# Optimization experiments

Hardware: AMD Instinct MI355X
Metric: run time of the kernel (lower is better)

Reference implementation:

```python
import jax, jax.numpy as jnp
import numpy as np

R = 0.5  # init kwarg r; reduction='mean'
N = 8192


def setup_inputs() -> dict:
    key = jax.random.key(0)
    k1, k2, k3 = jax.random.split(key, 3)
    pred = jax.random.normal(k1, (N, 1), dtype=jnp.float32)
    time = jax.random.uniform(k2, (N,), dtype=jnp.float32) * 100.0  # survival times
    event = jax.random.randint(k3, (N,), 0, 2).astype(jnp.float32)  # censoring indicator in {0,1}
    target = jnp.stack([time, event], axis=1)  # [N, 2]
    return {"pred": pred, "target": target}


def reference(pred, target):
    p = pred.squeeze(-1)            # [n]
    time = target[:, 0]             # [n]
    event = target[:, 1]            # [n]

    diff = p - time
    diff = jnp.where(event == 0, jnp.maximum(diff, 0.0), diff)
    regression_loss = jnp.mean(diff * diff)

    # ranking branch over all n^2 ordered pairs (i=index2 slow, j=index1 fast):
    # valid pair iff time[j] > time[i] and event[i] == 1
    mask = (time[None, :] > time[:, None]) & (event[:, None] == 1)  # [n, n] bool
    hinge = jnp.maximum(1.0 - p[None, :] + p[:, None], 0.0)         # [n, n]
    cnt = jnp.maximum(mask.sum(), 1).astype(jnp.float32)            # dynamic pair count -> masked mean
    ranking_loss = jnp.sum(jnp.where(mask, hinge * hinge, 0.0)) / cnt

    return R * ranking_loss + (1.0 - R) * regression_loss
```

## Files before the change

### kernel.cpp

```cpp
#include <hip/hip_runtime.h>

#define BLK 256
#define ITILE 256
#define KJ 2
#define JTILE (BLK * KJ)

__global__ __launch_bounds__(BLK) void svm_partial(
    const float* __restrict__ pred,
    const float2* __restrict__ tg,
    float* __restrict__ ws_rank,
    float* __restrict__ ws_reg,
    unsigned int* __restrict__ ws_cnt) {
  const int tid = threadIdx.x;
  const int i0 = blockIdx.x * ITILE;
  const int j0 = blockIdx.y * JTILE;

  float pj[KJ], tj[KJ];
  #pragma unroll
  for (int k = 0; k < KJ; ++k) {
    pj[k] = pred[j0 + tid + k * BLK];
    tj[k] = tg[j0 + tid + k * BLK].x;
  }

  float rank = 0.0f;
  unsigned int cnt = 0u;

  for (int ib = 0; ib < ITILE; ib += 8) {
    float pi[8], ti[8], ei[8];
    #pragma unroll
    for (int u = 0; u < 8; ++u) {
      pi[u] = pred[i0 + ib + u];
      float2 te = tg[i0 + ib + u];
      ti[u] = te.x;
      ei[u] = te.y;
    }
    #pragma unroll
    for (int u = 0; u < 8; ++u) {
      if (ei[u] == 1.0f) {
        const float pi1 = pi[u] + 1.0f;
        #pragma unroll
        for (int k = 0; k < KJ; ++k) {
          const float h = fmaxf(pi1 - pj[k], 0.0f);
          const bool m = tj[k] > ti[u];
          const float hm = m ? h : 0.0f;
          rank = fmaf(hm, hm, rank);
          cnt += m ? 1u : 0u;
        }
      }
    }
  }

  float reg = 0.0f;
  if (blockIdx.y == 0) {
    const int i = i0 + tid;
    const float p = pred[i];
    const float2 te = tg[i];
    float d = p - te.x;
    if (te.y == 0.0f) d = fmaxf(d, 0.0f);
    reg = d * d;
  }

  #pragma unroll
  for (int off = 32; off > 0; off >>= 1) {
    rank += __shfl_down(rank, off);
    reg  += __shfl_down(reg, off);
    cnt  += __shfl_down(cnt, off);
  }

  __shared__ float sr[BLK / 64];
  __shared__ float sg[BLK / 64];
  __shared__ unsigned int sc[BLK / 64];
  const int wave = tid >> 6;
  const int lane = tid & 63;
  if (lane == 0) { sr[wave] = rank; sg[wave] = reg; sc[wave] = cnt; }
  __syncthreads();

  if (tid == 0) {
    float r = 0.f, g = 0.f;
    unsigned int c = 0u;
    #pragma unroll
    for (int w = 0; w < BLK / 64; ++w) { r += sr[w]; g += sg[w]; c += sc[w]; }
    const int slot = blockIdx.y * gridDim.x + blockIdx.x;
    ws_rank[slot] = r;
    ws_reg[slot]  = g;
    ws_cnt[slot]  = c;
  }
}

__global__ __launch_bounds__(BLK) void svm_finalize(
    const float* __restrict__ ws_rank,
    const float* __restrict__ ws_reg,
    const unsigned int* __restrict__ ws_cnt,
    float* __restrict__ out, int n, int nslots) {
  const int tid = threadIdx.x;
  double r = 0.0, g = 0.0;
  unsigned long long c = 0ull;
  for (int s = tid; s < nslots; s += BLK) {
    r += (double)ws_rank[s];
    g += (double)ws_reg[s];
    c += (unsigned long long)ws_cnt[s];
  }
  #pragma unroll
  for (int off = 32; off > 0; off >>= 1) {
    r += __shfl_down(r, off);
    g += __shfl_down(g, off);
    c += __shfl_down(c, off);
  }
  __shared__ double dr[BLK / 64];
  __shared__ double dg[BLK / 64];
  __shared__ unsigned long long dc[BLK / 64];
  const int wave = tid >> 6;
  const int lane = tid & 63;
  if (lane == 0) { dr[wave] = r; dg[wave] = g; dc[wave] = c; }
  __syncthreads();
  if (tid == 0) {
    r = dr[0] + dr[1] + dr[2] + dr[3];
    g = dg[0] + dg[1] + dg[2] + dg[3];
    c = dc[0] + dc[1] + dc[2] + dc[3];
    const double cnt = (double)(c > 0ull ? c : 1ull);
    out[0] = (float)(0.5 * r / cnt + 0.5 * g / (double)n);
  }
}

extern "C" void kernel_launch(void* const* d_in, const int* in_sizes, int n_in,
                              void* d_out, int out_size, void* d_ws, size_t ws_size,
                              hipStream_t stream) {
  const float* pred = (const float*)d_in[0];
  const float2* tg = (const float2*)d_in[1];
  float* out = (float*)d_out;
  const int n = in_sizes[0];

  const int gx = n / ITILE;
  const int gy = n / JTILE;
  const int nslots = gx * gy;

  float* ws_rank = (float*)d_ws;
  float* ws_reg  = (float*)((char*)d_ws + nslots * sizeof(float));
  unsigned int* ws_cnt = (unsigned int*)((char*)d_ws + 2 * nslots * sizeof(float));

  dim3 grid(gx, gy);
  svm_partial<<<grid, BLK, 0, stream>>>(pred, tg, ws_rank, ws_reg, ws_cnt);
  svm_finalize<<<1, BLK, 0, stream>>>(ws_rank, ws_reg, ws_cnt, out, n, nslots);
}
```

Before: 73.09 us.

## Fuse partial and finalize kernels via cooperative launch with grid sync

Merges the pairwise partial-sum kernel and the single-block finalize kernel into one cooperative kernel. A grid-wide barrier separates the two phases, and block (0,0) then does the final reduction. This removes a second kernel launch and its gap, at the cost of cooperative-launch overhead and a grid barrier. The grid is also hardcoded to 32x16, which assumes N=8192.

```diff
diff --git a/kernel.cpp b/kernel.cpp
--- a/kernel.cpp
+++ b/kernel.cpp
@@ -1,16 +1,24 @@
 #include <hip/hip_runtime.h>
+#include <hip/hip_cooperative_groups.h>
+
+namespace cg = cooperative_groups;
 
 #define BLK 256
 #define ITILE 256
 #define KJ 2
 #define JTILE (BLK * KJ)
+#define GX 32
+#define GY 16
+#define NSLOTS (GX * GY)
 
-__global__ __launch_bounds__(BLK) void svm_partial(
+__global__ __launch_bounds__(BLK) void svm_fused(
     const float* __restrict__ pred,
     const float2* __restrict__ tg,
     float* __restrict__ ws_rank,
     float* __restrict__ ws_reg,
-    unsigned int* __restrict__ ws_cnt) {
+    unsigned int* __restrict__ ws_cnt,
+    float* __restrict__ out,
+    int n) {
   const int tid = threadIdx.x;
   const int i0 = blockIdx.x * ITILE;
   const int j0 = blockIdx.y * JTILE;
@@ -80,45 +88,40 @@
     unsigned int c = 0u;
     #pragma unroll
     for (int w = 0; w < BLK / 64; ++w) { r += sr[w]; g += sg[w]; c += sc[w]; }
-    const int slot = blockIdx.y * gridDim.x + blockIdx.x;
+    const int slot = blockIdx.y * GX + blockIdx.x;
     ws_rank[slot] = r;
     ws_reg[slot]  = g;
     ws_cnt[slot]  = c;
   }
-}
 
-__global__ __launch_bounds__(BLK) void svm_finalize(
-    const float* __restrict__ ws_rank,
-    const float* __restrict__ ws_reg,
-    const unsigned int* __restrict__ ws_cnt,
-    float* __restrict__ out, int n, int nslots) {
-  const int tid = threadIdx.x;
-  double r = 0.0, g = 0.0;
-  unsigned long long c = 0ull;
-  for (int s = tid; s < nslots; s += BLK) {
-    r += (double)ws_rank[s];
-    g += (double)ws_reg[s];
-    c += (unsigned long long)ws_cnt[s];
-  }
-  #pragma unroll
-  for (int off = 32; off > 0; off >>= 1) {
-    r += __shfl_down(r, off);
-    g += __shfl_down(g, off);
-    c += __shfl_down(c, off);
-  }
-  __shared__ double dr[BLK / 64];
-  __shared__ double dg[BLK / 64];
-  __shared__ unsigned long long dc[BLK / 64];
-  const int wave = tid >> 6;
-  const int lane = tid & 63;
-  if (lane == 0) { dr[wave] = r; dg[wave] = g; dc[wave] = c; }
-  __syncthreads();
-  if (tid == 0) {
-    r = dr[0] + dr[1] + dr[2] + dr[3];
-    g = dg[0] + dg[1] + dg[2] + dg[3];
-    c = dc[0] + dc[1] + dc[2] + dc[3];
-    const double cnt = (double)(c > 0ull ? c : 1ull);
-    out[0] = (float)(0.5 * r / cnt + 0.5 * g / (double)n);
+  cg::this_grid().sync();
+
+  if (blockIdx.x == 0 && blockIdx.y == 0) {
+    double r = 0.0, g = 0.0;
+    unsigned long long c = 0ull;
+    for (int s = tid; s < NSLOTS; s += BLK) {
+      r += (double)ws_rank[s];
+      g += (double)ws_reg[s];
+      c += (unsigned long long)ws_cnt[s];
+    }
+    #pragma unroll
+    for (int off = 32; off > 0; off >>= 1) {
+      r += __shfl_down(r, off);
+      g += __shfl_down(g, off);
+      c += __shfl_down(c, off);
+    }
+    __shared__ double dr[BLK / 64];
+    __shared__ double dg[BLK / 64];
+    __shared__ unsigned long long dc[BLK / 64];
+    if (lane == 0) { dr[wave] = r; dg[wave] = g; dc[wave] = c; }
+    __syncthreads();
+    if (tid == 0) {
+      r = dr[0] + dr[1] + dr[2] + dr[3];
+      g = dg[0] + dg[1] + dg[2] + dg[3];
+      c = dc[0] + dc[1] + dc[2] + dc[3];
+      const double cd = (double)(c > 0ull ? c : 1ull);
+      out[0] = (float)(0.5 * r / cd + 0.5 * g / (double)n);
+    }
   }
 }
 
@@ -128,17 +131,14 @@
   const float* pred = (const float*)d_in[0];
   const float2* tg = (const float2*)d_in[1];
   float* out = (float*)d_out;
-  const int n = in_sizes[0];
-
-  const int gx = n / ITILE;
-  const int gy = n / JTILE;
-  const int nslots = gx * gy;
+  int n = in_sizes[0];
 
   float* ws_rank = (float*)d_ws;
-  float* ws_reg  = (float*)((char*)d_ws + nslots * sizeof(float));
-  unsigned int* ws_cnt = (unsigned int*)((char*)d_ws + 2 * nslots * sizeof(float));
+  float* ws_reg  = (float*)((char*)d_ws + NSLOTS * sizeof(float));
+  unsigned int* ws_cnt = (unsigned int*)((char*)d_ws + 2 * NSLOTS * sizeof(float));
 
-  dim3 grid(gx, gy);
-  svm_partial<<<grid, BLK, 0, stream>>>(pred, tg, ws_rank, ws_reg, ws_cnt);
-  svm_finalize<<<1, BLK, 0, stream>>>(ws_rank, ws_reg, ws_cnt, out, n, nslots);
+  void* args[] = {(void*)&pred, (void*)&tg, (void*)&ws_rank, (void*)&ws_reg,
+                  (void*)&ws_cnt, (void*)&out, (void*)&n};
+  hipLaunchCooperativeKernel((const void*)svm_fused, dim3(GX, GY), dim3(BLK),
+                             args, 0, stream);
 }
```

Measured after the change: 127.6 us. 1.75x slower.
